# Kernel optimization log

Hardware: AMD Instinct MI355X
Metric: run time of the kernel (lower is better)

The kernel has to match this reference:

```python
import jax, jax.numpy as jnp
import numpy as np

N = 100000          # nodes
E = 1600000         # edges
D_NODE = 128        # num_node_features
D_EDGE = 128        # num_edge_features
OUT = 64            # out_features
HEADS = 2
HID = OUT * HEADS   # 128
NUM_GRAPHS = 64
NEG_SLOPE = 0.2


def setup_inputs() -> dict:
    key = jax.random.key(0)
    ks = jax.random.split(key, 12)
    glorot = lambda k, shape: jax.random.uniform(
        k, shape, jnp.float32, -1.0, 1.0) * np.sqrt(6.0 / (shape[0] + shape[-1]))
    return {
        "x": jax.random.normal(ks[0], (N, D_NODE), jnp.float32),
        "edge_index": jax.random.randint(ks[1], (2, E), 0, N, jnp.int64),
        "edge_attr": jax.random.normal(ks[2], (E, D_EDGE), jnp.float32),
        "batch": jnp.sort(jax.random.randint(ks[3], (N,), 0, NUM_GRAPHS, jnp.int64)),
        # GATConv params
        "lin_w": glorot(ks[4], (D_NODE, HID)),
        "att_src": glorot(ks[5], (HEADS, OUT)),
        "att_dst": glorot(ks[6], (HEADS, OUT)),
        "gat_bias": jnp.zeros((HID,), jnp.float32),
        # edge_lin params
        "edge_w": glorot(ks[7], (D_EDGE, HID)),
        "edge_b": jnp.zeros((HID,), jnp.float32),
        # MLP params
        "w1": glorot(ks[8], (HID, 32)),
        "b1": jnp.zeros((32,), jnp.float32),
        "w2": glorot(ks[9], (32, 1)),
        "b2": jnp.zeros((1,), jnp.float32),
    }


def reference(x, edge_index, edge_attr, batch, lin_w, att_src, att_dst,
              gat_bias, edge_w, edge_b, w1, b1, w2, b2):
    n = x.shape[0]
    # --- GATConv (concat=True, add_self_loops=True, negative_slope=0.2) ---
    h = (x @ lin_w).reshape(n, HEADS, OUT)                 # [N,H,C]
    loop = jnp.arange(n, dtype=edge_index.dtype)
    src = jnp.concatenate([edge_index[0], loop])           # [E+N]
    dst = jnp.concatenate([edge_index[1], loop])
    a_src = jnp.sum(h * att_src, axis=-1)                  # [N,H]
    a_dst = jnp.sum(h * att_dst, axis=-1)
    e = jax.nn.leaky_relu(a_src[src] + a_dst[dst], NEG_SLOPE)  # [E+N,H]
    e_max = jax.ops.segment_max(e, dst, num_segments=n)    # softmax over incoming edges
    e_exp = jnp.exp(e - e_max[dst])
    denom = jax.ops.segment_sum(e_exp, dst, num_segments=n)
    alpha = e_exp / (denom[dst] + 1e-16)                   # [E+N,H]
    msg = h[src] * alpha[:, :, None]                       # [E+N,H,C]
    node_feat = jax.ops.segment_sum(msg, dst, num_segments=n)
    node_feat = node_feat.reshape(n, HID) + gat_bias       # [N,HID]
    # --- edge features: linear + scatter-add to SOURCE node (the python loop) ---
    edge_feat = edge_attr @ edge_w + edge_b                # [E,HID]
    edge_agg = jax.ops.segment_sum(edge_feat, edge_index[0], num_segments=n)
    combined = node_feat + edge_agg                        # [N,HID]
    # --- global_add_pool + MLP ---
    pooled = jax.ops.segment_sum(combined, batch, num_segments=NUM_GRAPHS)
    return (pooled @ w1 + b1) @ w2 + b2                    # [NUM_GRAPHS,1]
```

## Files before the change

### kernel.cpp

```cpp
#include <hip/hip_runtime.h>
#include <hip/hip_bf16.h>
#include <math.h>


#define NG 64

typedef float f32x4 __attribute__((ext_vector_type(4)));

__device__ __forceinline__ float lrelu(float v){ return v > 0.f ? v : 0.2f*v; }

__global__ __launch_bounds__(256) void k_zero(float4* __restrict__ p, long long n4,
                                              int* __restrict__ nstart)
{
  long long i = (long long)blockIdx.x*256 + threadIdx.x;
  long long stride = (long long)gridDim.x*256;
  float4 z = make_float4(0.f,0.f,0.f,0.f);
  for (; i < n4; i += stride) p[i] = z;
  if (blockIdx.x == 0 && threadIdx.x < NG) nstart[threadIdx.x] = 0x7fffffff;
}

__global__ __launch_bounds__(256) void k_gemm_h(
    const float* __restrict__ x, const float* __restrict__ W,
    const float* __restrict__ att_src, const float* __restrict__ att_dst,
    float* __restrict__ h, float* __restrict__ aS, float* __restrict__ aD,
    float* __restrict__ denom, int N)
{
  __shared__ float ldsX[32*128];
  int rb = blockIdx.x * 32;
  for (int idx = threadIdx.x; idx < 32*128/4; idx += 256){
    int k = (idx*4) & 127;
    int row = rb + (idx >> 5);
    float4 v = make_float4(0.f,0.f,0.f,0.f);
    if (row < N) v = *(const float4*)&x[(size_t)row*128 + k];
    *(float4*)&ldsX[idx*4] = v;
  }
  __syncthreads();
  int ty = threadIdx.x >> 5, tx = threadIdx.x & 31;
  int r0 = ty*4, c0 = tx*4;
  float acc[4][4] = {};
  #pragma unroll 4
  for (int k = 0; k < 128; ++k){
    float4 b = *(const float4*)&W[k*128 + c0];
    float a0 = ldsX[(r0+0)*128 + k];
    float a1 = ldsX[(r0+1)*128 + k];
    float a2 = ldsX[(r0+2)*128 + k];
    float a3 = ldsX[(r0+3)*128 + k];
    acc[0][0] += a0*b.x; acc[0][1] += a0*b.y; acc[0][2] += a0*b.z; acc[0][3] += a0*b.w;
    acc[1][0] += a1*b.x; acc[1][1] += a1*b.y; acc[1][2] += a1*b.z; acc[1][3] += a1*b.w;
    acc[2][0] += a2*b.x; acc[2][1] += a2*b.y; acc[2][2] += a2*b.z; acc[2][3] += a2*b.w;
    acc[3][0] += a3*b.x; acc[3][1] += a3*b.y; acc[3][2] += a3*b.z; acc[3][3] += a3*b.w;
  }
  #pragma unroll
  for (int i=0;i<4;++i){
    int row = rb + r0 + i;
    if (row < N){
      float4 v = make_float4(acc[i][0],acc[i][1],acc[i][2],acc[i][3]);
      *(float4*)&h[(size_t)row*128 + c0] = v;
    }
  }
  float4 vs = *(const float4*)&att_src[c0];
  float4 vd = *(const float4*)&att_dst[c0];
  int head = tx >> 4;
  #pragma unroll
  for (int i=0;i<4;++i){
    float ps = acc[i][0]*vs.x + acc[i][1]*vs.y + acc[i][2]*vs.z + acc[i][3]*vs.w;
    float pd = acc[i][0]*vd.x + acc[i][1]*vd.y + acc[i][2]*vd.z + acc[i][3]*vd.w;
    ps += __shfl_xor(ps,1); ps += __shfl_xor(ps,2); ps += __shfl_xor(ps,4); ps += __shfl_xor(ps,8);
    pd += __shfl_xor(pd,1); pd += __shfl_xor(pd,2); pd += __shfl_xor(pd,4); pd += __shfl_xor(pd,8);
    if ((tx & 15) == 0){
      int row = rb + r0 + i;
      if (row < N){
        aS[row*2+head] = ps;
        aD[row*2+head] = pd;
        denom[row*2+head] = __expf(lrelu(ps+pd));
      }
    }
  }
}

__global__ __launch_bounds__(256) void k_deg_denom(
  const int* __restrict__ src, const int* __restrict__ dst,
  const float* __restrict__ aS, const float* __restrict__ aD,
  int* __restrict__ deg, float* __restrict__ denom, int E)
{
  int e = blockIdx.x*256 + threadIdx.x; if (e >= E) return;
  int s = src[e], d = dst[e];
  atomicAdd(&deg[s], 1);
  float2 as = *(const float2*)&aS[(size_t)s*2];
  float2 ad = *(const float2*)&aD[(size_t)d*2];
  atomicAdd(&denom[d*2+0], __expf(lrelu(as.x+ad.x)));
  atomicAdd(&denom[d*2+1], __expf(lrelu(as.y+ad.y)));
}

__global__ __launch_bounds__(256) void k_bsum(
  const int* __restrict__ deg, int* __restrict__ bsum, int N)
{
  __shared__ int s[256];
  int b = blockIdx.x, t = threadIdx.x, base = b*1024;
  int sum = 0;
  #pragma unroll
  for (int q=0;q<4;++q){ int i = base + t*4 + q; if (i < N) sum += deg[i]; }
  s[t] = sum; __syncthreads();
  for (int o=128;o;o>>=1){ if (t<o) s[t]+=s[t+o]; __syncthreads(); }
  if (t==0) bsum[b] = s[0];
}

__global__ void k_bscan(const int* __restrict__ bsum, int* __restrict__ boff,
                        int* __restrict__ doff, int nbk, int N, int E)
{
  if (threadIdx.x == 0){
    int s = 0;
    for (int b=0;b<nbk;++b){ boff[b]=s; s+=bsum[b]; }
    doff[N] = E;
  }
}

__global__ __launch_bounds__(256) void k_doff(
  const int* __restrict__ deg, const int* __restrict__ boff,
  int* __restrict__ doff, int* __restrict__ gpos, int N)
{
  __shared__ int s[256];
  int b = blockIdx.x, t = threadIdx.x, base = b*1024;
  int v[4]; int t4 = 0;
  #pragma unroll
  for (int q=0;q<4;++q){ int i = base + t*4 + q; v[q] = (i<N)?deg[i]:0; t4 += v[q]; }
  s[t] = t4; __syncthreads();
  for (int o=1;o<256;o<<=1){
    int add = (t>=o)? s[t-o] : 0;
    __syncthreads();
    s[t] += add;
    __syncthreads();
  }
  int run = boff[b] + s[t] - t4;
  #pragma unroll
  for (int q=0;q<4;++q){
    int i = base + t*4 + q;
    if (i < N){ doff[i] = run; gpos[i] = run; run += v[q]; }
  }
}

__global__ __launch_bounds__(256) void k_node_post(
  const float* __restrict__ aD, const float* __restrict__ denom,
  const int* __restrict__ batch, float4* __restrict__ adn,
  int* __restrict__ nstart, int N)
{
  int i = blockIdx.x*256 + threadIdx.x; if (i >= N) return;
  adn[i] = make_float4(aD[i*2], aD[i*2+1], denom[i*2], denom[i*2+1]);
  int b = batch[i];
  if (i == 0 || batch[i-1] != b) atomicMin(&nstart[b], i);
}

__global__ __launch_bounds__(256) void k_scatter(
  const int* __restrict__ src, const int* __restrict__ dst,
  const int* __restrict__ batch, int* __restrict__ gpos,
  int2* __restrict__ order2, const int* __restrict__ nstart,
  const int* __restrict__ doff, int* __restrict__ goff_e,
  float* __restrict__ cnt_nf, float* __restrict__ cnt_ef, int N, int E)
{
  if (blockIdx.x == 0 && threadIdx.x == 0){
    int arr[NG+1];
    arr[NG] = N;
    for (int g=NG-1; g>=0; --g){
      int v = nstart[g];
      arr[g] = (v <= N) ? v : arr[g+1];
    }
    for (int g=0; g<NG; ++g) goff_e[g] = doff[arr[g]];
    goff_e[NG] = E;
    for (int g=0; g<NG; ++g){
      cnt_nf[g] = (float)(arr[g+1]-arr[g]);
      cnt_ef[g] = (float)(goff_e[g+1]-goff_e[g]);
    }
  }
  int e = blockIdx.x*256 + threadIdx.x; if (e >= E) return;
  int s = src[e], d = dst[e];
  int gb = batch[d];
  int p = atomicAdd(&gpos[s], 1);
  order2[p] = make_int2(e, d | ((s & 63) << 17) | (gb << 23));
}

__global__ __launch_bounds__(256) void k_alpha_rows(
  const int2* __restrict__ order2, const int* __restrict__ doff,
  const float* __restrict__ aS, const float4* __restrict__ adn,
  const int* __restrict__ batch, float* __restrict__ P, int N)
{
  __shared__ float row[64*128];
  __shared__ float saS[128];
  __shared__ int sb[64];
  int s0 = blockIdx.x*64, t = threadIdx.x;
  for (int idx=t; idx<2048; idx+=256) ((float4*)row)[idx] = make_float4(0,0,0,0);
  if (t < 128){ int i = s0*2 + t; saS[t] = (i < 2*N) ? aS[i] : 0.f; }
  if (t < 64){ int i = s0 + t; sb[t] = (i < N) ? batch[i] : 0; }
  __syncthreads();
  int hi = s0 + 64; if (hi > N) hi = N;
  int i0 = doff[s0], i1 = doff[hi];
  for (int i = i0 + t; i < i1; i += 256){
    int y = order2[i].y;
    int d = y & 0x1FFFF;
    int lo = (y >> 17) & 63;
    int gb = (y >> 23) & 63;
    float4 q = adn[d];
    float a0 = __expf(lrelu(saS[lo*2+0] + q.x)) / (q.z + 1e-16f);
    float a1 = __expf(lrelu(saS[lo*2+1] + q.y)) / (q.w + 1e-16f);
    atomicAdd(&row[lo*128 + gb],      a0);
    atomicAdd(&row[lo*128 + 64 + gb], a1);
  }
  __syncthreads();
  if (t < 64){
    int s = s0 + t;
    if (s < N){
      float4 q = adn[s];
      row[t*128 + sb[t]]      += __expf(lrelu(saS[t*2+0] + q.x)) / (q.z + 1e-16f);
      row[t*128 + 64 + sb[t]] += __expf(lrelu(saS[t*2+1] + q.y)) / (q.w + 1e-16f);
    }
  }
  __syncthreads();
  for (int idx=t; idx<2048; idx+=256){
    int r = idx >> 5;
    int s = s0 + r;
    if (s < N) ((float4*)&P[(size_t)s*128])[idx & 31] = ((float4*)row)[idx];
  }
}

__global__ __launch_bounds__(256) void k_pgemm(
  const float* __restrict__ P, const float* __restrict__ h,
  float* __restrict__ partial, int N)
{
  __shared__ float sP[64*128];
  int t = threadIdx.x;
  int c = t & 127;
  int gh = t >> 7;
  int head = c >> 6;
  float acc[32];
  #pragma unroll
  for (int i=0;i<32;++i) acc[i] = 0.f;
  int j0 = blockIdx.x * 128;
  for (int sbi=0; sbi<2; ++sbi){
    int jb = j0 + sbi*64;
    __syncthreads();
    for (int idx=t; idx<2048; idx+=256){
      int j = jb + (idx >> 5);
      ((float4*)sP)[idx] = (j < N) ? ((const float4*)&P[(size_t)j*128])[idx & 31]
                                   : make_float4(0,0,0,0);
    }
    __syncthreads();
    for (int jj=0; jj<64; ++jj){
      int j = jb + jj;
      float hv = (j < N) ? h[(size_t)j*128 + c] : 0.f;
      const float* rp = &sP[jj*128 + head*64 + gh*32];
      #pragma unroll
      for (int q=0;q<8;++q){
        float4 pv = *(const float4*)&rp[q*4];
        acc[q*4+0] += pv.x*hv; acc[q*4+1] += pv.y*hv;
        acc[q*4+2] += pv.z*hv; acc[q*4+3] += pv.w*hv;
      }
    }
  }
  float* pb = &partial[(size_t)blockIdx.x*8192];
  #pragma unroll
  for (int i=0;i<32;++i) pb[(gh*32+i)*128 + c] = acc[i];
}

__global__ __launch_bounds__(256) void k_pg_reduce(
  const float* __restrict__ partial, float* __restrict__ pooled_gat, int nPB)
{
  int o = blockIdx.x*256 + threadIdx.x;
  int chunk = (nPB + gridDim.y - 1) / gridDim.y;
  int b0 = blockIdx.y * chunk;
  int b1 = b0 + chunk; if (b1 > nPB) b1 = nPB;
  float s = 0.f;
  for (int b=b0; b<b1; ++b) s += partial[(size_t)b*8192 + o];
  atomicAdd(&pooled_gat[o], s);
}

#define EA_SPLITS 64
__global__ __launch_bounds__(256) void k_eattr_sum(
  const float* __restrict__ ea, const int2* __restrict__ order2,
  const int* __restrict__ goff_e, float* __restrict__ pooled_e)
{
  __shared__ int sord[512];
  __shared__ float facc[128];
  int g = blockIdx.x / EA_SPLITS, k = blockIdx.x % EA_SPLITS;
  int start = goff_e[g], cnt = goff_e[g+1] - start;
  int len = (cnt + EA_SPLITS - 1) / EA_SPLITS;
  int i0 = start + k*len;
  int i1 = start + cnt; if (i0 + len < i1) i1 = i0 + len;
  int t = threadIdx.x, lane = t & 31, sub = t >> 5;
  const f32x4* ea4 = (const f32x4*)ea;
  f32x4 acc = {0.f,0.f,0.f,0.f};
  for (int base = i0; base < i1; base += 512){
    int m = i1 - base; if (m > 512) m = 512;
    __syncthreads();
    for (int idx = t; idx < m; idx += 256) sord[idx] = order2[base + idx].x;
    __syncthreads();
    int j = sub;
    for (; j + 56 < m; j += 64){
      f32x4 v0 = __builtin_nontemporal_load(&ea4[(size_t)sord[j     ]*32 + lane]);
      f32x4 v1 = __builtin_nontemporal_load(&ea4[(size_t)sord[j +  8]*32 + lane]);
      f32x4 v2 = __builtin_nontemporal_load(&ea4[(size_t)sord[j + 16]*32 + lane]);
      f32x4 v3 = __builtin_nontemporal_load(&ea4[(size_t)sord[j + 24]*32 + lane]);
      f32x4 v4 = __builtin_nontemporal_load(&ea4[(size_t)sord[j + 32]*32 + lane]);
      f32x4 v5 = __builtin_nontemporal_load(&ea4[(size_t)sord[j + 40]*32 + lane]);
      f32x4 v6 = __builtin_nontemporal_load(&ea4[(size_t)sord[j + 48]*32 + lane]);
      f32x4 v7 = __builtin_nontemporal_load(&ea4[(size_t)sord[j + 56]*32 + lane]);
      acc += (v0+v1)+(v2+v3)+((v4+v5)+(v6+v7));
    }
    for (; j < m; j += 8){
      f32x4 v = __builtin_nontemporal_load(&ea4[(size_t)sord[j]*32 + lane]);
      acc += v;
    }
  }
  if (t < 128) facc[t] = 0.f;
  __syncthreads();
  float* a = &facc[lane*4];
  atomicAdd(a+0, acc.x); atomicAdd(a+1, acc.y);
  atomicAdd(a+2, acc.z); atomicAdd(a+3, acc.w);
  __syncthreads();
  if (t < 128) atomicAdd(&pooled_e[g*128 + t], facc[t]);
}

__global__ __launch_bounds__(128) void k_final(
  const float* __restrict__ pooled_gat, const float* __restrict__ pooled_e,
  const float* __restrict__ cnt_nf, const float* __restrict__ cnt_ef,
  const float* __restrict__ gat_bias, const float* __restrict__ edge_w,
  const float* __restrict__ edge_b, const float* __restrict__ w1,
  const float* __restrict__ b1, const float* __restrict__ w2,
  const float* __restrict__ b2, float* __restrict__ out)
{
  __shared__ float lds_e[128], comb[128], t1[32];
  int g = blockIdx.x, c = threadIdx.x;
  lds_e[c] = pooled_e[g*128 + c];
  __syncthreads();
  float acc = pooled_gat[g*128 + c] + cnt_nf[g]*gat_bias[c] + cnt_ef[g]*edge_b[c];
  for (int k=0; k<128; ++k) acc += lds_e[k] * edge_w[k*128 + c];
  comb[c] = acc;
  __syncthreads();
  if (c < 32){
    float tv = b1[c];
    for (int k=0; k<128; ++k) tv += comb[k] * w1[k*32 + c];
    t1[c] = tv;
  }
  __syncthreads();
  if (c == 0){
    float o = b2[0];
    #pragma unroll
    for (int m=0; m<32; ++m) o += t1[m] * w2[m];
    out[g] = o;
  }
}

extern "C" void kernel_launch(void* const* d_in, const int* in_sizes, int n_in,
                              void* d_out, int out_size, void* d_ws, size_t ws_size,
                              hipStream_t stream) {
  const float* x        = (const float*)d_in[0];
  const int*   ei       = (const int*)d_in[1];
  const float* ea       = (const float*)d_in[2];
  const int*   batch    = (const int*)d_in[3];
  const float* lin_w    = (const float*)d_in[4];
  const float* att_src  = (const float*)d_in[5];
  const float* att_dst  = (const float*)d_in[6];
  const float* gat_bias = (const float*)d_in[7];
  const float* edge_w   = (const float*)d_in[8];
  const float* edge_b   = (const float*)d_in[9];
  const float* w1       = (const float*)d_in[10];
  const float* b1       = (const float*)d_in[11];
  const float* w2       = (const float*)d_in[12];
  const float* b2       = (const float*)d_in[13];
  float* out = (float*)d_out;

  int N = in_sizes[0] / 128;
  int E = in_sizes[1] / 2;
  const int* src = ei;
  const int* dst = ei + E;
  int nbk = (N + 1023) / 1024;
  int nPB = (N + 127) / 128;

  char* ws = (char*)d_ws;
  size_t off = 0;
  float* pooled_e   = (float*)(ws + off); off += (size_t)NG*128*4;
  float* pooled_gat = (float*)(ws + off); off += (size_t)NG*128*4;
  int*   deg        = (int*)  (ws + off); off += ((size_t)N*4 + 15) & ~15ull;
  size_t zero_bytes = off;
  float* h        = (float*)(ws + off); off += (size_t)N*128*4;
  float* P        = (float*)(ws + off); off += (size_t)N*128*4;
  float* partial  = (float*)(ws + off); off += (size_t)nPB*8192*4;
  float* aS       = (float*)(ws + off); off += (size_t)2*N*4;
  float* aD       = (float*)(ws + off); off += (size_t)2*N*4;
  float* denom    = (float*)(ws + off); off += (size_t)2*N*4;
  float4* adn     = (float4*)(ws + off); off += (size_t)N*16;
  int*   doff     = (int*)  (ws + off); off += ((size_t)(N+1)*4 + 15) & ~15ull;
  int*   gpos     = (int*)  (ws + off); off += ((size_t)N*4 + 15) & ~15ull;
  int2*  order2   = (int2*) (ws + off); off += (size_t)E*8;
  int*   bsum     = (int*)  (ws + off); off += 1024*4;
  int*   boff     = (int*)  (ws + off); off += 1024*4;
  int*   nstart   = (int*)  (ws + off); off += NG*4;
  int*   goff_e   = (int*)  (ws + off); off += (NG+1)*4;
  float* cnt_nf   = (float*)(ws + off); off += NG*4;
  float* cnt_ef   = (float*)(ws + off); off += NG*4;

  k_zero<<<128, 256, 0, stream>>>((float4*)d_ws, (long long)(zero_bytes/16), nstart);

  k_gemm_h   <<<(N+31)/32, 256, 0, stream>>>(x, lin_w, att_src, att_dst,
                                             h, aS, aD, denom, N);
  k_deg_denom<<<(E+255)/256, 256, 0, stream>>>(src, dst, aS, aD, deg, denom, E);

  k_bsum     <<<nbk, 256, 0, stream>>>(deg, bsum, N);
  k_bscan    <<<1, 1, 0, stream>>>(bsum, boff, doff, nbk, N, E);
  k_doff     <<<nbk, 256, 0, stream>>>(deg, boff, doff, gpos, N);
  k_node_post<<<(N+255)/256, 256, 0, stream>>>(aD, denom, batch, adn, nstart, N);
  k_scatter  <<<(E+255)/256, 256, 0, stream>>>(src, dst, batch, gpos, order2,
                                               nstart, doff, goff_e,
                                               cnt_nf, cnt_ef, N, E);

  k_alpha_rows<<<(N+63)/64, 256, 0, stream>>>(order2, doff, aS, adn, batch, P, N);
  k_pgemm     <<<nPB, 256, 0, stream>>>(P, h, partial, N);
  {
    dim3 rg(32, 8);
    k_pg_reduce<<<rg, 256, 0, stream>>>(partial, pooled_gat, nPB);
  }

  k_eattr_sum<<<NG*EA_SPLITS, 256, 0, stream>>>(ea, order2, goff_e, pooled_e);

  k_final<<<NG, 128, 0, stream>>>(pooled_gat, pooled_e, cnt_nf, cnt_ef,
                                  gat_bias, edge_w, edge_b, w1, b1, w2, b2, out);
}
```

Measured before the change: 676.7 us.

## Merge edge-attr pooling into alpha-row kernel and fold node_post into doff

Horizontally fuses the edge-attribute gather-sum into the alpha-row kernel: the first NG*EA_SPLITS blocks do edge-attr pooling and the rest build the alpha rows, so the bandwidth-heavy edge_attr stream overlaps with the alpha scatter work. The node post-processing (packing adn and the graph-start atomics) is folded into the doff prefix-scan kernel, which removes a launch. The x loads in the first GEMM become nontemporal. The fused kernel's shared-memory footprint now applies to the edge-attr blocks too, which may limit occupancy for those blocks.

```diff
diff --git a/kernel.cpp b/kernel.cpp
--- a/kernel.cpp
+++ b/kernel.cpp
@@ -4,6 +4,7 @@
 
 
 #define NG 64
+#define EA_SPLITS 64
 
 typedef float f32x4 __attribute__((ext_vector_type(4)));
 
@@ -30,9 +31,9 @@
   for (int idx = threadIdx.x; idx < 32*128/4; idx += 256){
     int k = (idx*4) & 127;
     int row = rb + (idx >> 5);
-    float4 v = make_float4(0.f,0.f,0.f,0.f);
-    if (row < N) v = *(const float4*)&x[(size_t)row*128 + k];
-    *(float4*)&ldsX[idx*4] = v;
+    f32x4 v = {0.f,0.f,0.f,0.f};
+    if (row < N) v = __builtin_nontemporal_load((const f32x4*)&x[(size_t)row*128 + k]);
+    *(f32x4*)&ldsX[idx*4] = v;
   }
   __syncthreads();
   int ty = threadIdx.x >> 5, tx = threadIdx.x & 31;
@@ -117,7 +118,10 @@
 
 __global__ __launch_bounds__(256) void k_doff(
   const int* __restrict__ deg, const int* __restrict__ boff,
-  int* __restrict__ doff, int* __restrict__ gpos, int N)
+  int* __restrict__ doff, int* __restrict__ gpos,
+  const float* __restrict__ aD, const float* __restrict__ denom,
+  const int* __restrict__ batch, float4* __restrict__ adn,
+  int* __restrict__ nstart, int N)
 {
   __shared__ int s[256];
   int b = blockIdx.x, t = threadIdx.x, base = b*1024;
@@ -135,19 +139,13 @@
   #pragma unroll
   for (int q=0;q<4;++q){
     int i = base + t*4 + q;
-    if (i < N){ doff[i] = run; gpos[i] = run; run += v[q]; }
-  }
-}
-
-__global__ __launch_bounds__(256) void k_node_post(
-  const float* __restrict__ aD, const float* __restrict__ denom,
-  const int* __restrict__ batch, float4* __restrict__ adn,
-  int* __restrict__ nstart, int N)
-{
-  int i = blockIdx.x*256 + threadIdx.x; if (i >= N) return;
-  adn[i] = make_float4(aD[i*2], aD[i*2+1], denom[i*2], denom[i*2+1]);
-  int b = batch[i];
-  if (i == 0 || batch[i-1] != b) atomicMin(&nstart[b], i);
+    if (i < N){
+      doff[i] = run; gpos[i] = run; run += v[q];
+      adn[i] = make_float4(aD[i*2], aD[i*2+1], denom[i*2], denom[i*2+1]);
+      int bb = batch[i];
+      if (i == 0 || batch[i-1] != bb) atomicMin(&nstart[bb], i);
+    }
+  }
 }
 
 __global__ __launch_bounds__(256) void k_scatter(
@@ -178,15 +176,62 @@
   order2[p] = make_int2(e, d | ((s & 63) << 17) | (gb << 23));
 }
 
-__global__ __launch_bounds__(256) void k_alpha_rows(
+__global__ __launch_bounds__(256) void k_alpha_eattr(
   const int2* __restrict__ order2, const int* __restrict__ doff,
   const float* __restrict__ aS, const float4* __restrict__ adn,
-  const int* __restrict__ batch, float* __restrict__ P, int N)
+  const int* __restrict__ batch, float* __restrict__ P,
+  const float* __restrict__ ea, const int* __restrict__ goff_e,
+  float* __restrict__ pooled_e, int N, int nEA)
 {
   __shared__ float row[64*128];
   __shared__ float saS[128];
   __shared__ int sb[64];
-  int s0 = blockIdx.x*64, t = threadIdx.x;
+  int t = threadIdx.x;
+
+  if ((int)blockIdx.x < nEA){
+    int* sord = (int*)row;
+    float* facc = row + 1024;
+    int g = blockIdx.x / EA_SPLITS, k = blockIdx.x % EA_SPLITS;
+    int start = goff_e[g], cnt = goff_e[g+1] - start;
+    int len = (cnt + EA_SPLITS - 1) / EA_SPLITS;
+    int i0 = start + k*len;
+    int i1 = start + cnt; if (i0 + len < i1) i1 = i0 + len;
+    int lane = t & 31, sub = t >> 5;
+    const f32x4* ea4 = (const f32x4*)ea;
+    f32x4 acc = {0.f,0.f,0.f,0.f};
+    for (int base = i0; base < i1; base += 512){
+      int m = i1 - base; if (m > 512) m = 512;
+      __syncthreads();
+      for (int idx = t; idx < m; idx += 256) sord[idx] = order2[base + idx].x;
+      __syncthreads();
+      int j = sub;
+      for (; j + 56 < m; j += 64){
+        f32x4 v0 = __builtin_nontemporal_load(&ea4[(size_t)sord[j     ]*32 + lane]);
+        f32x4 v1 = __builtin_nontemporal_load(&ea4[(size_t)sord[j +  8]*32 + lane]);
+        f32x4 v2 = __builtin_nontemporal_load(&ea4[(size_t)sord[j + 16]*32 + lane]);
+        f32x4 v3 = __builtin_nontemporal_load(&ea4[(size_t)sord[j + 24]*32 + lane]);
+        f32x4 v4 = __builtin_nontemporal_load(&ea4[(size_t)sord[j + 32]*32 + lane]);
+        f32x4 v5 = __builtin_nontemporal_load(&ea4[(size_t)sord[j + 40]*32 + lane]);
+        f32x4 v6 = __builtin_nontemporal_load(&ea4[(size_t)sord[j + 48]*32 + lane]);
+        f32x4 v7 = __builtin_nontemporal_load(&ea4[(size_t)sord[j + 56]*32 + lane]);
+        acc += (v0+v1)+(v2+v3)+((v4+v5)+(v6+v7));
+      }
+      for (; j < m; j += 8){
+        acc += __builtin_nontemporal_load(&ea4[(size_t)sord[j]*32 + lane]);
+      }
+    }
+    __syncthreads();
+    if (t < 128) facc[t] = 0.f;
+    __syncthreads();
+    float* a = &facc[lane*4];
+    atomicAdd(a+0, acc.x); atomicAdd(a+1, acc.y);
+    atomicAdd(a+2, acc.z); atomicAdd(a+3, acc.w);
+    __syncthreads();
+    if (t < 128) atomicAdd(&pooled_e[g*128 + t], facc[t]);
+    return;
+  }
+
+  int s0 = ((int)blockIdx.x - nEA)*64;
   for (int idx=t; idx<2048; idx+=256) ((float4*)row)[idx] = make_float4(0,0,0,0);
   if (t < 128){ int i = s0*2 + t; saS[t] = (i < 2*N) ? aS[i] : 0.f; }
   if (t < 64){ int i = s0 + t; sb[t] = (i < N) ? batch[i] : 0; }
@@ -270,52 +315,6 @@
   float s = 0.f;
   for (int b=b0; b<b1; ++b) s += partial[(size_t)b*8192 + o];
   atomicAdd(&pooled_gat[o], s);
-}
-
-#define EA_SPLITS 64
-__global__ __launch_bounds__(256) void k_eattr_sum(
-  const float* __restrict__ ea, const int2* __restrict__ order2,
-  const int* __restrict__ goff_e, float* __restrict__ pooled_e)
-{
-  __shared__ int sord[512];
-  __shared__ float facc[128];
-  int g = blockIdx.x / EA_SPLITS, k = blockIdx.x % EA_SPLITS;
-  int start = goff_e[g], cnt = goff_e[g+1] - start;
-  int len = (cnt + EA_SPLITS - 1) / EA_SPLITS;
-  int i0 = start + k*len;
-  int i1 = start + cnt; if (i0 + len < i1) i1 = i0 + len;
-  int t = threadIdx.x, lane = t & 31, sub = t >> 5;
-  const f32x4* ea4 = (const f32x4*)ea;
-  f32x4 acc = {0.f,0.f,0.f,0.f};
-  for (int base = i0; base < i1; base += 512){
-    int m = i1 - base; if (m > 512) m = 512;
-    __syncthreads();
-    for (int idx = t; idx < m; idx += 256) sord[idx] = order2[base + idx].x;
-    __syncthreads();
-    int j = sub;
-    for (; j + 56 < m; j += 64){
-      f32x4 v0 = __builtin_nontemporal_load(&ea4[(size_t)sord[j     ]*32 + lane]);
-      f32x4 v1 = __builtin_nontemporal_load(&ea4[(size_t)sord[j +  8]*32 + lane]);
-      f32x4 v2 = __builtin_nontemporal_load(&ea4[(size_t)sord[j + 16]*32 + lane]);
-      f32x4 v3 = __builtin_nontemporal_load(&ea4[(size_t)sord[j + 24]*32 + lane]);
-      f32x4 v4 = __builtin_nontemporal_load(&ea4[(size_t)sord[j + 32]*32 + lane]);
-      f32x4 v5 = __builtin_nontemporal_load(&ea4[(size_t)sord[j + 40]*32 + lane]);
-      f32x4 v6 = __builtin_nontemporal_load(&ea4[(size_t)sord[j + 48]*32 + lane]);
-      f32x4 v7 = __builtin_nontemporal_load(&ea4[(size_t)sord[j + 56]*32 + lane]);
-      acc += (v0+v1)+(v2+v3)+((v4+v5)+(v6+v7));
-    }
-    for (; j < m; j += 8){
-      f32x4 v = __builtin_nontemporal_load(&ea4[(size_t)sord[j]*32 + lane]);
-      acc += v;
-    }
-  }
-  if (t < 128) facc[t] = 0.f;
-  __syncthreads();
-  float* a = &facc[lane*4];
-  atomicAdd(a+0, acc.x); atomicAdd(a+1, acc.y);
-  atomicAdd(a+2, acc.z); atomicAdd(a+3, acc.w);
-  __syncthreads();
-  if (t < 128) atomicAdd(&pooled_e[g*128 + t], facc[t]);
 }
 
 __global__ __launch_bounds__(128) void k_final(
@@ -373,6 +372,8 @@
   const int* dst = ei + E;
   int nbk = (N + 1023) / 1024;
   int nPB = (N + 127) / 128;
+  int nAB = (N + 63) / 64;
+  int nEA = NG * EA_SPLITS;
 
   char* ws = (char*)d_ws;
   size_t off = 0;
@@ -405,21 +406,21 @@
 
   k_bsum     <<<nbk, 256, 0, stream>>>(deg, bsum, N);
   k_bscan    <<<1, 1, 0, stream>>>(bsum, boff, doff, nbk, N, E);
-  k_doff     <<<nbk, 256, 0, stream>>>(deg, boff, doff, gpos, N);
-  k_node_post<<<(N+255)/256, 256, 0, stream>>>(aD, denom, batch, adn, nstart, N);
+  k_doff     <<<nbk, 256, 0, stream>>>(deg, boff, doff, gpos,
+                                       aD, denom, batch, adn, nstart, N);
   k_scatter  <<<(E+255)/256, 256, 0, stream>>>(src, dst, batch, gpos, order2,
                                                nstart, doff, goff_e,
                                                cnt_nf, cnt_ef, N, E);
 
-  k_alpha_rows<<<(N+63)/64, 256, 0, stream>>>(order2, doff, aS, adn, batch, P, N);
-  k_pgemm     <<<nPB, 256, 0, stream>>>(P, h, partial, N);
+  k_alpha_eattr<<<nEA + nAB, 256, 0, stream>>>(order2, doff, aS, adn, batch, P,
+                                               ea, goff_e, pooled_e, N, nEA);
+
+  k_pgemm    <<<nPB, 256, 0, stream>>>(P, h, partial, N);
   {
     dim3 rg(32, 8);
     k_pg_reduce<<<rg, 256, 0, stream>>>(partial, pooled_gat, nPB);
   }
 
-  k_eattr_sum<<<NG*EA_SPLITS, 256, 0, stream>>>(ea, order2, goff_e, pooled_e);
-
   k_final<<<NG, 128, 0, stream>>>(pooled_gat, pooled_e, cnt_nf, cnt_ef,
                                   gat_bias, edge_w, edge_b, w1, b1, w2, b2, out);
 }
```

New measurement: 657.9 us, median of 2. 2.8% less time.
